# Kernel tuning notes

Measured on AMD Instinct MI355X. Metric: run time of the kernel, lower is better.

Reference implementation:

```python
import jax, jax.numpy as jnp
import numpy as np

EPS = 1e-6

def setup_inputs() -> dict:
    key = jax.random.key(0)
    kq, kk, kv = jax.random.split(key, 3)
    B, N, D = 4, 4096, 1024
    Q = jax.random.normal(kq, (B, N, D), dtype=jnp.float32)
    K = jax.random.normal(kk, (B, N, D), dtype=jnp.float32)
    V = jax.random.normal(kv, (B, N, D), dtype=jnp.float32)
    return {"Q": Q, "K": K, "V": V}

def reference(Q, K, V):
    # phi(x) = elu(x) + 1
    phi = lambda x: jax.nn.elu(x) + 1.0
    Q_phi = phi(Q)                                   # [B,N,D]
    K_phi = phi(K)                                   # [B,N,D]
    K_sum = K_phi.sum(axis=1)                        # [B,D]
    Z = jnp.einsum('bnd,bd->bn', Q_phi, K_sum) + EPS # [B,N]
    KV = jnp.einsum('bnd,bne->bde', K_phi, V)        # [B,D,E]
    context = jnp.einsum('bnd,bde->bne', Q_phi, KV)  # [B,N,E]
    out = context / Z[..., None]
    return out  # dropout is identity at inference (rate set to 0)
```

## Files before the change

kernel.cpp:

```cpp
#include <hip/hip_runtime.h>

#define BATCH 4
#define SEQ   4096
#define DIM   1024
#define EPS_F 1e-6f
#define KSPLIT 4

typedef __bf16 bf16_t;
typedef bf16_t bf16x8 __attribute__((ext_vector_type(8)));
typedef float  f32x4  __attribute__((ext_vector_type(4)));
typedef unsigned short u16x8 __attribute__((ext_vector_type(8)));

__device__ __forceinline__ unsigned short f2bf(float f) {
  unsigned u = __float_as_uint(f);
  u += 0x7FFFu + ((u >> 16) & 1u);
  return (unsigned short)(u >> 16);
}
__device__ __forceinline__ float bf2f(unsigned short h) {
  return __uint_as_float(((unsigned)h) << 16);
}
__device__ __forceinline__ float phi_f(float x) {
  return x > 0.f ? x + 1.f : __expf(x);
}

__global__ __launch_bounds__(256) void zero_f32(float* __restrict__ p, int n) {
  const int i = blockIdx.x * 256 + threadIdx.x;
  if (i < n) p[i] = 0.f;
}

template<bool PHI, bool KSUM>
__global__ __launch_bounds__(256) void phi_transpose(const float* __restrict__ in,
    unsigned short* __restrict__ out, float* __restrict__ ksum, int rows, int cols) {
  __shared__ float t[32][33];
  __shared__ float ps[8][32];
  const int bx = blockIdx.x * 32;
  const int by = blockIdx.y * 32;
  const size_t bo = (size_t)blockIdx.z * rows * cols;
  const int x = threadIdx.x, y = threadIdx.y;
  #pragma unroll
  for (int j = 0; j < 32; j += 8) {
    float v = in[bo + (size_t)(by + y + j) * cols + bx + x];
    if (PHI) v = phi_f(v);
    t[y + j][x] = v;
  }
  __syncthreads();
  #pragma unroll
  for (int j = 0; j < 32; j += 8)
    out[bo + (size_t)(bx + y + j) * rows + by + x] = f2bf(t[x][y + j]);
  if (KSUM) {
    float s = t[y][x] + t[y + 8][x] + t[y + 16][x] + t[y + 24][x];
    ps[y][x] = s;
    __syncthreads();
    if (y == 0) {
      float tot = 0.f;
      #pragma unroll
      for (int j = 0; j < 8; ++j) tot += ps[j][x];
      atomicAdd(&ksum[(size_t)blockIdx.z * cols + bx + x], tot);
    }
  }
}

__global__ __launch_bounds__(256) void phi_cast_qz(const float* __restrict__ Q,
    const float* __restrict__ Ksum, unsigned short* __restrict__ Qp,
    float* __restrict__ invZ) {
  const int row  = blockIdx.x * 4 + (threadIdx.x >> 6);
  const int lane = threadIdx.x & 63;
  const int b = row >> 12;
  const float* q  = Q + (size_t)row * DIM;
  const float* ks = Ksum + (size_t)b * DIM;
  float s = 0.f;
  #pragma unroll
  for (int c = 0; c < 2; ++c) {
    const int d0 = c * 512 + lane * 8;
    float4 v0 = *(const float4*)(q + d0);
    float4 v1 = *(const float4*)(q + d0 + 4);
    float4 k0 = *(const float4*)(ks + d0);
    float4 k1 = *(const float4*)(ks + d0 + 4);
    u16x8 o;
    o[0] = f2bf(phi_f(v0.x)); s += bf2f(o[0]) * k0.x;
    o[1] = f2bf(phi_f(v0.y)); s += bf2f(o[1]) * k0.y;
    o[2] = f2bf(phi_f(v0.z)); s += bf2f(o[2]) * k0.z;
    o[3] = f2bf(phi_f(v0.w)); s += bf2f(o[3]) * k0.w;
    o[4] = f2bf(phi_f(v1.x)); s += bf2f(o[4]) * k1.x;
    o[5] = f2bf(phi_f(v1.y)); s += bf2f(o[5]) * k1.y;
    o[6] = f2bf(phi_f(v1.z)); s += bf2f(o[6]) * k1.z;
    o[7] = f2bf(phi_f(v1.w)); s += bf2f(o[7]) * k1.w;
    *(u16x8*)(Qp + (size_t)row * DIM + d0) = o;
  }
  #pragma unroll
  for (int off = 32; off > 0; off >>= 1) s += __shfl_down(s, off);
  if (lane == 0) invZ[row] = 1.0f / (s + EPS_F);
}

__global__ __launch_bounds__(256) void reduce_kv(const unsigned short* __restrict__ P,
    unsigned short* __restrict__ KVt) {
  const size_t per = (size_t)DIM * DIM;
  const size_t i = ((size_t)blockIdx.x * 256 + threadIdx.x) * 8;
  const size_t b = blockIdx.y;
  const unsigned short* p = P + b * KSPLIT * per + i;
  float s[8] = {};
  #pragma unroll
  for (int sp = 0; sp < KSPLIT; ++sp) {
    u16x8 v = *(const u16x8*)(p + sp * per);
    #pragma unroll
    for (int j = 0; j < 8; ++j) s[j] += bf2f(v[j]);
  }
  u16x8 o;
  #pragma unroll
  for (int j = 0; j < 8; ++j) o[j] = f2bf(s[j]);
  *(u16x8*)(KVt + b * per + i) = o;
}

#define GLD(gp, lp) __builtin_amdgcn_global_load_lds( \
    (const __attribute__((address_space(1))) unsigned int*)(gp), \
    (__attribute__((address_space(3))) unsigned int*)(lp), 16, 0, 0)
#define BARRIER __builtin_amdgcn_s_barrier()
#define WAITV(n) asm volatile("s_waitcnt vmcnt(" #n ")" ::: "memory")

template<int EPI, int KS, int NT>
__global__ __launch_bounds__(512, 2) void gemm256_bt(
    const unsigned short* __restrict__ A, const unsigned short* __restrict__ Bm,
    void* __restrict__ Cv, const float* __restrict__ invZ,
    int M, int Nc, int K, int gx, int gy) {
  extern __shared__ unsigned short lds[];
  unsigned short* const As0 = lds;
  unsigned short* const As1 = lds + 16384;
  unsigned short* const Bs0 = lds + 32768;
  unsigned short* const Bs1 = lds + 49152;

  const int t    = threadIdx.x;
  const int wid  = t >> 6;
  const int lane = t & 63;
  const int id   = blockIdx.x;
  const int sw   = (id & 7) * (gridDim.x >> 3) + (id >> 3);
  const int bxi  = sw % gx;
  const int rem  = sw / gx;
  const int byi  = rem % gy;
  const int bz   = rem / gy;
  const int brow = byi * 256, bcol = bxi * 256;
  const size_t batch = bz / KS;
  const int split = bz % KS;
  const int Kc = K / KS;
  const unsigned short* Ab = A + batch * ((size_t)M * K) + (size_t)brow * K + (size_t)split * Kc;
  const unsigned short* Bb = Bm + batch * ((size_t)Nc * K) + (size_t)bcol * K + (size_t)split * Kc;

  const int srow_t = t >> 3;
  const int c_src  = (t & 7) ^ (srow_t & 7);
  const unsigned short* gA = Ab + (size_t)srow_t * K + c_src * 8;
  const unsigned short* gB = Bb + (size_t)((srow_t >> 5) * 64 + (srow_t & 31)) * K + c_src * 8;
  const int ldsAu = wid * 512;
  const int ldsBu = wid * 512 + (wid >> 2) * 2048;

  auto stageA = [&](unsigned short* D, int h, int kt) {
    GLD(gA + (size_t)(h * 64) * K + (size_t)kt * 64,       D + (h * 64) * 64 + ldsAu);
    GLD(gA + (size_t)(128 + h * 64) * K + (size_t)kt * 64, D + (128 + h * 64) * 64 + ldsAu);
  };
  auto stageB = [&](unsigned short* D, int h, int kt) {
    GLD(gB + (size_t)(h * 32) * K + (size_t)kt * 64,       D + (h * 32) * 64 + ldsBu);
    GLD(gB + (size_t)(128 + h * 32) * K + (size_t)kt * 64, D + (128 + h * 32) * 64 + ldsBu);
  };

  const int fr  = lane & 15;
  const int g   = lane >> 4;
  const int wrw = (wid >> 2) * 128;
  const int wcw = (wid & 3) * 64;
  const int ck0 = ((g)     ^ (fr & 7)) * 8;
  const int ck1 = ((4 + g) ^ (fr & 7)) * 8;

  f32x4 acc[8][4] = {};
  bf16x8 afX[4][2], afY[4][2], bfX[2][2], bfY[2][2];

#define LDA(S, mh, DST) { _Pragma("unroll") for (int m_ = 0; m_ < 4; ++m_) { \
    const int ro_ = (wrw + ((mh) * 4 + m_) * 16 + fr) * 64; \
    DST[m_][0] = *(const bf16x8*)((S) + ro_ + ck0); \
    DST[m_][1] = *(const bf16x8*)((S) + ro_ + ck1); } }
#define LDBF(S, nh, DST) { _Pragma("unroll") for (int n_ = 0; n_ < 2; ++n_) { \
    const int ro_ = (wcw + (nh) * 32 + n_ * 16 + fr) * 64; \
    DST[n_][0] = *(const bf16x8*)((S) + ro_ + ck0); \
    DST[n_][1] = *(const bf16x8*)((S) + ro_ + ck1); } }
#define MM(mh, nh, AF, BF) { __builtin_amdgcn_s_setprio(1); \
    _Pragma("unroll") for (int m_ = 0; m_ < 4; ++m_) \
    _Pragma("unroll") for (int n_ = 0; n_ < 2; ++n_) \
    _Pragma("unroll") for (int k_ = 0; k_ < 2; ++k_) \
      acc[(mh) * 4 + m_][(nh) * 2 + n_] = __builtin_amdgcn_mfma_f32_16x16x32_bf16( \
          AF[m_][k_], BF[n_][k_], acc[(mh) * 4 + m_][(nh) * 2 + n_], 0, 0, 0); \
    __builtin_amdgcn_s_setprio(0); }

  unsigned short *Ac = As0, *An = As1, *Bc = Bs0, *Bn = Bs1;

  stageA(Ac, 0, 0); stageB(Bc, 0, 0); stageB(Bc, 1, 0); stageA(Ac, 1, 0);
  stageA(An, 0, 1); stageB(Bn, 0, 1); stageB(Bn, 1, 1);
  stageA(An, 1, 1);
  WAITV(8);
  BARRIER;
  LDA(Ac, 0, afX); LDBF(Bc, 0, bfX);

  #pragma unroll 1
  for (int it = 0; it < NT - 2; ++it) {
    const int t2 = it + 2;
    LDBF(Bc, 1, bfY);
    stageA(Ac, 0, t2);
    BARRIER; MM(0, 0, afX, bfX); BARRIER;
    stageB(Bc, 0, t2);
    WAITV(6);
    BARRIER;
    LDA(Ac, 1, afY);
    MM(0, 1, afX, bfY); BARRIER;
    LDA(An, 0, afX);
    stageB(Bc, 1, t2);
    BARRIER; MM(1, 0, afY, bfX); BARRIER;
    LDBF(Bn, 0, bfX);
    stageA(Ac, 1, t2);
    BARRIER; MM(1, 1, afY, bfY); BARRIER;
    unsigned short* tp;
    tp = Ac; Ac = An; An = tp;
    tp = Bc; Bc = Bn; Bn = tp;
  }
  LDBF(Bc, 1, bfY);
  BARRIER; MM(0, 0, afX, bfX); BARRIER;
  WAITV(0);
  BARRIER;
  LDA(Ac, 1, afY);
  MM(0, 1, afX, bfY); BARRIER;
  LDA(An, 0, afX);
  BARRIER; MM(1, 0, afY, bfX); BARRIER;
  LDBF(Bn, 0, bfX);
  BARRIER; MM(1, 1, afY, bfY); BARRIER;
  {
    unsigned short* tp;
    tp = Ac; Ac = An; An = tp;
    tp = Bc; Bc = Bn; Bn = tp;
  }
  LDBF(Bc, 1, bfY);
  BARRIER; MM(0, 0, afX, bfX);
  LDA(Ac, 1, afY);
  MM(0, 1, afX, bfY);
  MM(1, 0, afY, bfX);
  MM(1, 1, afY, bfY);
#undef LDA
#undef LDBF
#undef MM

  if (EPI == 0) {
    unsigned short* Cb = (unsigned short*)Cv + (size_t)bz * M * Nc;
    #pragma unroll
    for (int m = 0; m < 8; ++m) {
      const int row = brow + wrw + m * 16 + g * 4;
      #pragma unroll
      for (int r = 0; r < 4; ++r)
        #pragma unroll
        for (int n = 0; n < 4; ++n)
          Cb[(size_t)(row + r) * Nc + bcol + wcw + n * 16 + fr] = f2bf(acc[m][n][r]);
    }
  } else {
    float* Cb = (float*)Cv + batch * ((size_t)M * Nc);
    const float* zb = invZ + batch * (size_t)M;
    #pragma unroll
    for (int m = 0; m < 8; ++m) {
      const int row = brow + wrw + m * 16 + g * 4;
      #pragma unroll
      for (int r = 0; r < 4; ++r) {
        const float z = zb[row + r];
        #pragma unroll
        for (int n = 0; n < 4; ++n)
          Cb[(size_t)(row + r) * Nc + bcol + wcw + n * 16 + fr] = acc[m][n][r] * z;
      }
    }
  }
}

extern "C" void kernel_launch(void* const* d_in, const int* in_sizes, int n_in,
                              void* d_out, int out_size, void* d_ws, size_t ws_size,
                              hipStream_t stream) {
  const float* Q = (const float*)d_in[0];
  const float* K = (const float*)d_in[1];
  const float* V = (const float*)d_in[2];
  float* out = (float*)d_out;

  char* ws = (char*)d_ws;
  size_t off = 0;
  auto alloc = [&](size_t bytes) {
    void* p = ws + off;
    off += (bytes + 255) & ~(size_t)255;
    return p;
  };
  unsigned short* Qp   = (unsigned short*)alloc((size_t)BATCH * SEQ * DIM * 2);
  unsigned short* P    = Qp;
  unsigned short* Kt   = (unsigned short*)alloc((size_t)BATCH * SEQ * DIM * 2);
  unsigned short* Vt   = (unsigned short*)alloc((size_t)BATCH * SEQ * DIM * 2);
  unsigned short* KVt  = (unsigned short*)alloc((size_t)BATCH * DIM * DIM * 2);
  float* Ksum = (float*)alloc((size_t)BATCH * DIM * 4);
  float* invZ = (float*)alloc((size_t)BATCH * SEQ * 4);

  hipFuncSetAttribute(reinterpret_cast<const void*>(&gemm256_bt<0, KSPLIT, 16>),
                      hipFuncAttributeMaxDynamicSharedMemorySize, 131072);
  hipFuncSetAttribute(reinterpret_cast<const void*>(&gemm256_bt<1, 1, 16>),
                      hipFuncAttributeMaxDynamicSharedMemorySize, 131072);

  const dim3 tb(32, 8);
  zero_f32<<<(BATCH * DIM + 255) / 256, 256, 0, stream>>>(Ksum, BATCH * DIM);
  phi_transpose<true, true ><<<dim3(DIM / 32, SEQ / 32, BATCH), tb, 0, stream>>>(K, Kt, Ksum, SEQ, DIM);
  phi_transpose<false, false><<<dim3(DIM / 32, SEQ / 32, BATCH), tb, 0, stream>>>(V, Vt, nullptr, SEQ, DIM);
  gemm256_bt<0, KSPLIT, 16><<<(DIM / 256) * (DIM / 256) * BATCH * KSPLIT, 512, 131072, stream>>>(
      Vt, Kt, P, nullptr, DIM, DIM, SEQ, DIM / 256, DIM / 256);
  reduce_kv<<<dim3(DIM * DIM / (256 * 8), BATCH), 256, 0, stream>>>(P, KVt);
  phi_cast_qz<<<BATCH * SEQ / 4, 256, 0, stream>>>(Q, Ksum, Qp, invZ);
  gemm256_bt<1, 1, 16><<<(DIM / 256) * (SEQ / 256) * BATCH, 512, 131072, stream>>>(
      Qp, KVt, out, invZ, SEQ, DIM, DIM, DIM / 256, SEQ / 256);
}
```

Baseline: 146.7 us.

## Fuse Q phi/bf16 conversion and normalizer into the second GEMM

Removes the separate phi_cast_qz pass. The second GEMM now loads fp32 Q directly, applies phi, converts to bf16 into LDS, and computes the Z normalizer in-kernel from a Ksum copy held in LDS. This avoids writing and re-reading the bf16 Qp buffer and drops one launch. In exchange, each of the 4 column tiles recomputes phi and Z for its rows and reads twice as many bytes of Q per tile. It also runs at occupancy 1 with extra LDS and more complex interleaving.

```diff
diff --git a/kernel.cpp b/kernel.cpp
--- a/kernel.cpp
+++ b/kernel.cpp
@@ -60,38 +60,6 @@
   }
 }
 
-__global__ __launch_bounds__(256) void phi_cast_qz(const float* __restrict__ Q,
-    const float* __restrict__ Ksum, unsigned short* __restrict__ Qp,
-    float* __restrict__ invZ) {
-  const int row  = blockIdx.x * 4 + (threadIdx.x >> 6);
-  const int lane = threadIdx.x & 63;
-  const int b = row >> 12;
-  const float* q  = Q + (size_t)row * DIM;
-  const float* ks = Ksum + (size_t)b * DIM;
-  float s = 0.f;
-  #pragma unroll
-  for (int c = 0; c < 2; ++c) {
-    const int d0 = c * 512 + lane * 8;
-    float4 v0 = *(const float4*)(q + d0);
-    float4 v1 = *(const float4*)(q + d0 + 4);
-    float4 k0 = *(const float4*)(ks + d0);
-    float4 k1 = *(const float4*)(ks + d0 + 4);
-    u16x8 o;
-    o[0] = f2bf(phi_f(v0.x)); s += bf2f(o[0]) * k0.x;
-    o[1] = f2bf(phi_f(v0.y)); s += bf2f(o[1]) * k0.y;
-    o[2] = f2bf(phi_f(v0.z)); s += bf2f(o[2]) * k0.z;
-    o[3] = f2bf(phi_f(v0.w)); s += bf2f(o[3]) * k0.w;
-    o[4] = f2bf(phi_f(v1.x)); s += bf2f(o[4]) * k1.x;
-    o[5] = f2bf(phi_f(v1.y)); s += bf2f(o[5]) * k1.y;
-    o[6] = f2bf(phi_f(v1.z)); s += bf2f(o[6]) * k1.z;
-    o[7] = f2bf(phi_f(v1.w)); s += bf2f(o[7]) * k1.w;
-    *(u16x8*)(Qp + (size_t)row * DIM + d0) = o;
-  }
-  #pragma unroll
-  for (int off = 32; off > 0; off >>= 1) s += __shfl_down(s, off);
-  if (lane == 0) invZ[row] = 1.0f / (s + EPS_F);
-}
-
 __global__ __launch_bounds__(256) void reduce_kv(const unsigned short* __restrict__ P,
     unsigned short* __restrict__ KVt) {
   const size_t per = (size_t)DIM * DIM;
@@ -116,6 +84,7 @@
     (__attribute__((address_space(3))) unsigned int*)(lp), 16, 0, 0)
 #define BARRIER __builtin_amdgcn_s_barrier()
 #define WAITV(n) asm volatile("s_waitcnt vmcnt(" #n ")" ::: "memory")
+#define LGK(n)   asm volatile("s_waitcnt lgkmcnt(" #n ")" ::: "memory")
 
 template<int EPI, int KS, int NT>
 __global__ __launch_bounds__(512, 2) void gemm256_bt(
@@ -269,6 +238,192 @@
   }
 }
 
+__global__ __launch_bounds__(512, 1) void gemm2f(
+    const float* __restrict__ Qf, const unsigned short* __restrict__ Bm,
+    float* __restrict__ C, const float* __restrict__ KsumG) {
+  extern __shared__ unsigned short lds[];
+  unsigned short* const As0 = lds;
+  unsigned short* const As1 = lds + 16384;
+  unsigned short* const Bs0 = lds + 32768;
+  unsigned short* const Bs1 = lds + 49152;
+  float* const ksumL = (float*)(lds + 65536);
+  float* const zbuf  = (float*)(lds + 32768);
+  float* const zfin  = ((float*)(lds + 32768)) + 2048;
+
+  const int t    = threadIdx.x;
+  const int wid  = t >> 6;
+  const int lane = t & 63;
+  const int id   = blockIdx.x;
+  const int sw   = (id & 7) * (gridDim.x >> 3) + (id >> 3);
+  const int bxi  = sw % 4;
+  const int rem  = sw / 4;
+  const int byi  = rem % 16;
+  const int bz   = rem / 16;
+  const int brow = byi * 256, bcol = bxi * 256;
+  const float*          Ab = Qf + (size_t)bz * SEQ * DIM + (size_t)brow * DIM;
+  const unsigned short* Bb = Bm + (size_t)bz * DIM * DIM + (size_t)bcol * DIM;
+
+  const int srow  = t >> 3;
+  const int c_src = (t & 7) ^ (srow & 7);
+  const float* gQ = Ab + (size_t)srow * DIM + c_src * 8;
+  const unsigned short* gB = Bb + (size_t)((srow >> 5) * 64 + (srow & 31)) * DIM + c_src * 8;
+  const int ldsBu = wid * 512 + (wid >> 2) * 2048;
+  const int aoff  = srow * 64 + (t & 7) * 8;
+
+  auto stageB = [&](unsigned short* D, int h, int kt) {
+    GLD(gB + (size_t)(h * 32) * DIM + (size_t)kt * 64,       D + (h * 32) * 64 + ldsBu);
+    GLD(gB + (size_t)(128 + h * 32) * DIM + (size_t)kt * 64, D + (128 + h * 32) * 64 + ldsBu);
+  };
+
+  const int fr  = lane & 15;
+  const int g   = lane >> 4;
+  const int wrw = (wid >> 2) * 128;
+  const int wcw = (wid & 3) * 64;
+  const int ck0 = ((g)     ^ (fr & 7)) * 8;
+  const int ck1 = ((4 + g) ^ (fr & 7)) * 8;
+
+  f32x4 acc[8][4] = {};
+  bf16x8 af[4][2], bf0[2][2], bf1[2][2];
+  float4 sA0, sA1, sA2, sA3, sB0, sB1, sB2, sB3;
+  float zp0 = 0.f, zp1 = 0.f, zp2 = 0.f, zp3 = 0.f;
+
+#define LOADA(S, mh) { _Pragma("unroll") for (int m_ = 0; m_ < 4; ++m_) { \
+    const int ro_ = (wrw + ((mh) * 4 + m_) * 16 + fr) * 64; \
+    af[m_][0] = *(const bf16x8*)((S) + ro_ + ck0); \
+    af[m_][1] = *(const bf16x8*)((S) + ro_ + ck1); } }
+#define LOADB(S, nh, BF) { _Pragma("unroll") for (int n_ = 0; n_ < 2; ++n_) { \
+    const int ro_ = (wcw + (nh) * 32 + n_ * 16 + fr) * 64; \
+    BF[n_][0] = *(const bf16x8*)((S) + ro_ + ck0); \
+    BF[n_][1] = *(const bf16x8*)((S) + ro_ + ck1); } }
+#define QUAD(mh, nh, BF) { __builtin_amdgcn_s_setprio(1); \
+    _Pragma("unroll") for (int m_ = 0; m_ < 4; ++m_) \
+    _Pragma("unroll") for (int n_ = 0; n_ < 2; ++n_) \
+    _Pragma("unroll") for (int k_ = 0; k_ < 2; ++k_) \
+      acc[(mh) * 4 + m_][(nh) * 2 + n_] = __builtin_amdgcn_mfma_f32_16x16x32_bf16( \
+          af[m_][k_], BF[n_][k_], acc[(mh) * 4 + m_][(nh) * 2 + n_], 0, 0, 0); \
+    __builtin_amdgcn_s_setprio(0); }
+#define ISSUEQ(P, h, kt) { \
+    P##0 = *(const float4*)(gQ + (size_t)((h) * 64) * DIM + (kt) * 64); \
+    P##1 = *(const float4*)(gQ + (size_t)((h) * 64) * DIM + (kt) * 64 + 4); \
+    P##2 = *(const float4*)(gQ + (size_t)((h) * 64 + 128) * DIM + (kt) * 64); \
+    P##3 = *(const float4*)(gQ + (size_t)((h) * 64 + 128) * DIM + (kt) * 64 + 4); }
+#define CVT8(VA, VB, OUT, ZP, K0, K1) { u16x8 o_; float q_; \
+    o_[0] = f2bf(phi_f(VA.x)); q_ = bf2f(o_[0]); ZP += q_ * K0.x; \
+    o_[1] = f2bf(phi_f(VA.y)); q_ = bf2f(o_[1]); ZP += q_ * K0.y; \
+    o_[2] = f2bf(phi_f(VA.z)); q_ = bf2f(o_[2]); ZP += q_ * K0.z; \
+    o_[3] = f2bf(phi_f(VA.w)); q_ = bf2f(o_[3]); ZP += q_ * K0.w; \
+    o_[4] = f2bf(phi_f(VB.x)); q_ = bf2f(o_[4]); ZP += q_ * K1.x; \
+    o_[5] = f2bf(phi_f(VB.y)); q_ = bf2f(o_[5]); ZP += q_ * K1.y; \
+    o_[6] = f2bf(phi_f(VB.z)); q_ = bf2f(o_[6]); ZP += q_ * K1.z; \
+    o_[7] = f2bf(phi_f(VB.w)); q_ = bf2f(o_[7]); ZP += q_ * K1.w; \
+    OUT = o_; }
+#define COMMITQ(P, D, h, kt, ZA, ZB) { \
+    float4 kv0 = *(const float4*)(ksumL + (kt) * 64 + c_src * 8); \
+    float4 kv1 = *(const float4*)(ksumL + (kt) * 64 + c_src * 8 + 4); \
+    u16x8 w0, w1; \
+    CVT8(P##0, P##1, w0, ZA, kv0, kv1); \
+    CVT8(P##2, P##3, w1, ZB, kv0, kv1); \
+    *(u16x8*)((D) + ((h) * 64) * 64 + aoff)         = w0; \
+    *(u16x8*)((D) + ((h) * 64 + 128) * 64 + aoff)   = w1; }
+
+  if (t < 128) {
+    float4 k0 = *(const float4*)(KsumG + (size_t)bz * DIM + t * 8);
+    float4 k1 = *(const float4*)(KsumG + (size_t)bz * DIM + t * 8 + 4);
+    *(float4*)(ksumL + t * 8) = k0;
+    *(float4*)(ksumL + t * 8 + 4) = k1;
+  }
+  __syncthreads();
+
+  ISSUEQ(sA, 0, 0);
+  ISSUEQ(sB, 1, 0);
+  stageB(Bs0, 0, 0); stageB(Bs0, 1, 0);
+  COMMITQ(sA, As0, 0, 0, zp0, zp2);
+  COMMITQ(sB, As0, 1, 0, zp1, zp3);
+  ISSUEQ(sA, 0, 1);
+  stageB(Bs1, 0, 1); stageB(Bs1, 1, 1);
+  COMMITQ(sA, As1, 0, 1, zp0, zp2);
+  LGK(0);
+  BARRIER;
+
+  #pragma unroll 1
+  for (int i = 0; i < 7; ++i) {
+    const int k2 = 2 * i;
+    LOADA(As0, 0); LOADB(Bs0, 0, bf0); ISSUEQ(sA, 1, k2 + 1);
+    BARRIER; QUAD(0, 0, bf0); BARRIER;
+    LOADB(Bs0, 1, bf1); ISSUEQ(sB, 0, k2 + 2);
+    BARRIER; QUAD(0, 1, bf1);
+    COMMITQ(sA, As1, 1, k2 + 1, zp1, zp3); LGK(0); BARRIER;
+    LOADA(As0, 1); stageB(Bs0, 0, k2 + 2);
+    BARRIER; QUAD(1, 0, bf0);
+    COMMITQ(sB, As0, 0, k2 + 2, zp0, zp2); LGK(0); BARRIER;
+    stageB(Bs0, 1, k2 + 2);
+    BARRIER; QUAD(1, 1, bf1); BARRIER;
+    LOADA(As1, 0); LOADB(Bs1, 0, bf0); ISSUEQ(sA, 1, k2 + 2);
+    BARRIER; QUAD(0, 0, bf0); BARRIER;
+    LOADB(Bs1, 1, bf1); ISSUEQ(sB, 0, k2 + 3);
+    BARRIER; QUAD(0, 1, bf1);
+    COMMITQ(sA, As0, 1, k2 + 2, zp1, zp3); LGK(0); BARRIER;
+    LOADA(As1, 1); stageB(Bs1, 0, k2 + 3);
+    BARRIER; QUAD(1, 0, bf0);
+    COMMITQ(sB, As1, 0, k2 + 3, zp0, zp2); LGK(0); BARRIER;
+    stageB(Bs1, 1, k2 + 3);
+    BARRIER; QUAD(1, 1, bf1); BARRIER;
+  }
+  {
+    LOADA(As0, 0); LOADB(Bs0, 0, bf0); ISSUEQ(sA, 1, 15);
+    BARRIER; QUAD(0, 0, bf0); BARRIER;
+    LOADB(Bs0, 1, bf1);
+    BARRIER; QUAD(0, 1, bf1);
+    COMMITQ(sA, As1, 1, 15, zp1, zp3); LGK(0); BARRIER;
+    LOADA(As0, 1);
+    BARRIER; QUAD(1, 0, bf0); BARRIER;
+    BARRIER; QUAD(1, 1, bf1); BARRIER;
+    LOADA(As1, 0); LOADB(Bs1, 0, bf0);
+    BARRIER; QUAD(0, 0, bf0); BARRIER;
+    LOADB(Bs1, 1, bf1);
+    BARRIER; QUAD(0, 1, bf1); BARRIER;
+    LOADA(As1, 1);
+    BARRIER; QUAD(1, 0, bf0); BARRIER;
+    QUAD(1, 1, bf1);
+  }
+#undef LOADA
+#undef LOADB
+#undef QUAD
+#undef ISSUEQ
+#undef CVT8
+#undef COMMITQ
+
+  BARRIER;
+  zbuf[(srow)       * 8 + (t & 7)] = zp0;
+  zbuf[(srow + 64)  * 8 + (t & 7)] = zp1;
+  zbuf[(srow + 128) * 8 + (t & 7)] = zp2;
+  zbuf[(srow + 192) * 8 + (t & 7)] = zp3;
+  LGK(0);
+  BARRIER;
+  if (t < 256) {
+    float4 a = *(const float4*)(zbuf + t * 8);
+    float4 b = *(const float4*)(zbuf + t * 8 + 4);
+    const float s = a.x + a.y + a.z + a.w + b.x + b.y + b.z + b.w;
+    zfin[t] = 1.0f / (s + EPS_F);
+  }
+  LGK(0);
+  BARRIER;
+
+  float* Cb = C + (size_t)bz * SEQ * DIM;
+  #pragma unroll
+  for (int m = 0; m < 8; ++m) {
+    const int rl = wrw + m * 16 + g * 4;
+    #pragma unroll
+    for (int r = 0; r < 4; ++r) {
+      const float z = zfin[rl + r];
+      const int row = brow + rl + r;
+      #pragma unroll
+      for (int n = 0; n < 4; ++n)
+        Cb[(size_t)row * DIM + bcol + wcw + n * 16 + fr] = acc[m][n][r] * z;
+    }
+  }
+}
+
 extern "C" void kernel_launch(void* const* d_in, const int* in_sizes, int n_in,
                               void* d_out, int out_size, void* d_ws, size_t ws_size,
                               hipStream_t stream) {
@@ -284,18 +439,16 @@
     off += (bytes + 255) & ~(size_t)255;
     return p;
   };
-  unsigned short* Qp   = (unsigned short*)alloc((size_t)BATCH * SEQ * DIM * 2);
-  unsigned short* P    = Qp;
+  unsigned short* P    = (unsigned short*)alloc((size_t)BATCH * KSPLIT * DIM * DIM * 2);
   unsigned short* Kt   = (unsigned short*)alloc((size_t)BATCH * SEQ * DIM * 2);
   unsigned short* Vt   = (unsigned short*)alloc((size_t)BATCH * SEQ * DIM * 2);
   unsigned short* KVt  = (unsigned short*)alloc((size_t)BATCH * DIM * DIM * 2);
   float* Ksum = (float*)alloc((size_t)BATCH * DIM * 4);
-  float* invZ = (float*)alloc((size_t)BATCH * SEQ * 4);
 
   hipFuncSetAttribute(reinterpret_cast<const void*>(&gemm256_bt<0, KSPLIT, 16>),
                       hipFuncAttributeMaxDynamicSharedMemorySize, 131072);
-  hipFuncSetAttribute(reinterpret_cast<const void*>(&gemm256_bt<1, 1, 16>),
-                      hipFuncAttributeMaxDynamicSharedMemorySize, 131072);
+  hipFuncSetAttribute(reinterpret_cast<const void*>(&gemm2f),
+                      hipFuncAttributeMaxDynamicSharedMemorySize, 135168);
 
   const dim3 tb(32, 8);
   zero_f32<<<(BATCH * DIM + 255) / 256, 256, 0, stream>>>(Ksum, BATCH * DIM);
@@ -304,7 +457,5 @@
   gemm256_bt<0, KSPLIT, 16><<<(DIM / 256) * (DIM / 256) * BATCH * KSPLIT, 512, 131072, stream>>>(
       Vt, Kt, P, nullptr, DIM, DIM, SEQ, DIM / 256, DIM / 256);
   reduce_kv<<<dim3(DIM * DIM / (256 * 8), BATCH), 256, 0, stream>>>(P, KVt);
-  phi_cast_qz<<<BATCH * SEQ / 4, 256, 0, stream>>>(Q, Ksum, Qp, invZ);
-  gemm256_bt<1, 1, 16><<<(DIM / 256) * (SEQ / 256) * BATCH, 512, 131072, stream>>>(
-      Qp, KVt, out, invZ, SEQ, DIM, DIM, DIM / 256, SEQ / 256);
-}
+  gemm2f<<<4 * 16 * BATCH, 512, 135168, stream>>>(Q, KVt, out, Ksum);
+}
```

Measured after the change: 251.5 us. 1.71x slower.

## Restructure 256x256 GEMM to 16 waves with simpler double-buffered loop

Applied to the files above, without the earlier changes.

Rewrites the bf16 GEMM to run 1024 threads (16 waves) per 256x256 tile, so each wave owns a 64x64 sub-tile with half the accumulators. The finely interleaved half-tile pipeline is replaced by one pass per k-step: read fragments, wait on all LDS and global loads, barrier, issue the next stage, then run all MFMAs. The intent is more waves to hide latency and lower per-wave register pressure. The cost is more LDS fragment reads per MFMA and full waitcnt(0) stalls each iteration. The zero kernel is also replaced with hipMemsetAsync.

```diff
diff --git a/kernel.cpp b/kernel.cpp
--- a/kernel.cpp
+++ b/kernel.cpp
@@ -23,15 +23,10 @@
   return x > 0.f ? x + 1.f : __expf(x);
 }
 
-__global__ __launch_bounds__(256) void zero_f32(float* __restrict__ p, int n) {
-  const int i = blockIdx.x * 256 + threadIdx.x;
-  if (i < n) p[i] = 0.f;
-}
-
 template<bool PHI, bool KSUM>
 __global__ __launch_bounds__(256) void phi_transpose(const float* __restrict__ in,
     unsigned short* __restrict__ out, float* __restrict__ ksum, int rows, int cols) {
-  __shared__ float t[32][33];
+  __shared__ float tl[32][33];
   __shared__ float ps[8][32];
   const int bx = blockIdx.x * 32;
   const int by = blockIdx.y * 32;
@@ -41,14 +36,14 @@
   for (int j = 0; j < 32; j += 8) {
     float v = in[bo + (size_t)(by + y + j) * cols + bx + x];
     if (PHI) v = phi_f(v);
-    t[y + j][x] = v;
+    tl[y + j][x] = v;
   }
   __syncthreads();
   #pragma unroll
   for (int j = 0; j < 32; j += 8)
-    out[bo + (size_t)(bx + y + j) * rows + by + x] = f2bf(t[x][y + j]);
+    out[bo + (size_t)(bx + y + j) * rows + by + x] = f2bf(tl[x][y + j]);
   if (KSUM) {
-    float s = t[y][x] + t[y + 8][x] + t[y + 16][x] + t[y + 24][x];
+    float s = tl[y][x] + tl[y + 8][x] + tl[y + 16][x] + tl[y + 24][x];
     ps[y][x] = s;
     __syncthreads();
     if (y == 0) {
@@ -116,9 +111,10 @@
     (__attribute__((address_space(3))) unsigned int*)(lp), 16, 0, 0)
 #define BARRIER __builtin_amdgcn_s_barrier()
 #define WAITV(n) asm volatile("s_waitcnt vmcnt(" #n ")" ::: "memory")
+#define LGK(n)   asm volatile("s_waitcnt lgkmcnt(" #n ")" ::: "memory")
 
 template<int EPI, int KS, int NT>
-__global__ __launch_bounds__(512, 2) void gemm256_bt(
+__global__ __launch_bounds__(1024, 4) void gemm16w(
     const unsigned short* __restrict__ A, const unsigned short* __restrict__ Bm,
     void* __restrict__ Cv, const float* __restrict__ invZ,
     int M, int Nc, int K, int gx, int gy) {
@@ -144,107 +140,85 @@
   const unsigned short* Ab = A + batch * ((size_t)M * K) + (size_t)brow * K + (size_t)split * Kc;
   const unsigned short* Bb = Bm + batch * ((size_t)Nc * K) + (size_t)bcol * K + (size_t)split * Kc;
 
-  const int srow_t = t >> 3;
-  const int c_src  = (t & 7) ^ (srow_t & 7);
-  const unsigned short* gA = Ab + (size_t)srow_t * K + c_src * 8;
-  const unsigned short* gB = Bb + (size_t)((srow_t >> 5) * 64 + (srow_t & 31)) * K + c_src * 8;
-  const int ldsAu = wid * 512;
-  const int ldsBu = wid * 512 + (wid >> 2) * 2048;
-
-  auto stageA = [&](unsigned short* D, int h, int kt) {
-    GLD(gA + (size_t)(h * 64) * K + (size_t)kt * 64,       D + (h * 64) * 64 + ldsAu);
-    GLD(gA + (size_t)(128 + h * 64) * K + (size_t)kt * 64, D + (128 + h * 64) * 64 + ldsAu);
+  const int srow  = t >> 3;
+  const int c_src = (t & 7) ^ (srow & 7);
+  const unsigned short* gA = Ab + (size_t)srow * K + c_src * 8;
+  const unsigned short* gB = Bb + (size_t)srow * K + c_src * 8;
+  const int ldsu = wid * 512;
+
+  auto stageA = [&](unsigned short* D, int kt) {
+    GLD(gA + (size_t)kt * 64,                  D + ldsu);
+    GLD(gA + (size_t)128 * K + (size_t)kt * 64, D + 8192 + ldsu);
   };
-  auto stageB = [&](unsigned short* D, int h, int kt) {
-    GLD(gB + (size_t)(h * 32) * K + (size_t)kt * 64,       D + (h * 32) * 64 + ldsBu);
-    GLD(gB + (size_t)(128 + h * 32) * K + (size_t)kt * 64, D + (128 + h * 32) * 64 + ldsBu);
+  auto stageB = [&](unsigned short* D, int kt) {
+    GLD(gB + (size_t)kt * 64,                  D + ldsu);
+    GLD(gB + (size_t)128 * K + (size_t)kt * 64, D + 8192 + ldsu);
   };
 
   const int fr  = lane & 15;
   const int g   = lane >> 4;
-  const int wrw = (wid >> 2) * 128;
+  const int wrw = (wid >> 2) * 64;
   const int wcw = (wid & 3) * 64;
   const int ck0 = ((g)     ^ (fr & 7)) * 8;
   const int ck1 = ((4 + g) ^ (fr & 7)) * 8;
 
-  f32x4 acc[8][4] = {};
-  bf16x8 afX[4][2], afY[4][2], bfX[2][2], bfY[2][2];
-
-#define LDA(S, mh, DST) { _Pragma("unroll") for (int m_ = 0; m_ < 4; ++m_) { \
-    const int ro_ = (wrw + ((mh) * 4 + m_) * 16 + fr) * 64; \
-    DST[m_][0] = *(const bf16x8*)((S) + ro_ + ck0); \
-    DST[m_][1] = *(const bf16x8*)((S) + ro_ + ck1); } }
-#define LDBF(S, nh, DST) { _Pragma("unroll") for (int n_ = 0; n_ < 2; ++n_) { \
-    const int ro_ = (wcw + (nh) * 32 + n_ * 16 + fr) * 64; \
-    DST[n_][0] = *(const bf16x8*)((S) + ro_ + ck0); \
-    DST[n_][1] = *(const bf16x8*)((S) + ro_ + ck1); } }
-#define MM(mh, nh, AF, BF) { __builtin_amdgcn_s_setprio(1); \
+  f32x4 acc[4][4] = {};
+  bf16x8 af[4][2], bfr[4][2];
+
+#define READS(SA, SB) { \
+    _Pragma("unroll") for (int m_ = 0; m_ < 4; ++m_) { \
+      const int ro_ = (wrw + m_ * 16 + fr) * 64; \
+      af[m_][0] = *(const bf16x8*)((SA) + ro_ + ck0); \
+      af[m_][1] = *(const bf16x8*)((SA) + ro_ + ck1); } \
+    _Pragma("unroll") for (int n_ = 0; n_ < 4; ++n_) { \
+      const int ro_ = (wcw + n_ * 16 + fr) * 64; \
+      bfr[n_][0] = *(const bf16x8*)((SB) + ro_ + ck0); \
+      bfr[n_][1] = *(const bf16x8*)((SB) + ro_ + ck1); } }
+#define MMALL { __builtin_amdgcn_s_setprio(1); \
     _Pragma("unroll") for (int m_ = 0; m_ < 4; ++m_) \
-    _Pragma("unroll") for (int n_ = 0; n_ < 2; ++n_) \
+    _Pragma("unroll") for (int n_ = 0; n_ < 4; ++n_) \
     _Pragma("unroll") for (int k_ = 0; k_ < 2; ++k_) \
-      acc[(mh) * 4 + m_][(nh) * 2 + n_] = __builtin_amdgcn_mfma_f32_16x16x32_bf16( \
-          AF[m_][k_], BF[n_][k_], acc[(mh) * 4 + m_][(nh) * 2 + n_], 0, 0, 0); \
+      acc[m_][n_] = __builtin_amdgcn_mfma_f32_16x16x32_bf16( \
+          af[m_][k_], bfr[n_][k_], acc[m_][n_], 0, 0, 0); \
     __builtin_amdgcn_s_setprio(0); }
 
   unsigned short *Ac = As0, *An = As1, *Bc = Bs0, *Bn = Bs1;
 
-  stageA(Ac, 0, 0); stageB(Bc, 0, 0); stageB(Bc, 1, 0); stageA(Ac, 1, 0);
-  stageA(An, 0, 1); stageB(Bn, 0, 1); stageB(Bn, 1, 1);
-  stageA(An, 1, 1);
-  WAITV(8);
+  stageA(Ac, 0); stageB(Bc, 0);
+  stageA(An, 1); stageB(Bn, 1);
+  WAITV(4);
   BARRIER;
-  LDA(Ac, 0, afX); LDBF(Bc, 0, bfX);
 
   #pragma unroll 1
-  for (int it = 0; it < NT - 2; ++it) {
-    const int t2 = it + 2;
-    LDBF(Bc, 1, bfY);
-    stageA(Ac, 0, t2);
-    BARRIER; MM(0, 0, afX, bfX); BARRIER;
-    stageB(Bc, 0, t2);
-    WAITV(6);
+  for (int kt = 0; kt < NT - 2; ++kt) {
+    READS(Ac, Bc);
+    LGK(0);
+    WAITV(0);
     BARRIER;
-    LDA(Ac, 1, afY);
-    MM(0, 1, afX, bfY); BARRIER;
-    LDA(An, 0, afX);
-    stageB(Bc, 1, t2);
-    BARRIER; MM(1, 0, afY, bfX); BARRIER;
-    LDBF(Bn, 0, bfX);
-    stageA(Ac, 1, t2);
-    BARRIER; MM(1, 1, afY, bfY); BARRIER;
+    stageA(Ac, kt + 2); stageB(Bc, kt + 2);
+    MMALL;
     unsigned short* tp;
     tp = Ac; Ac = An; An = tp;
     tp = Bc; Bc = Bn; Bn = tp;
   }
-  LDBF(Bc, 1, bfY);
-  BARRIER; MM(0, 0, afX, bfX); BARRIER;
-  WAITV(0);
-  BARRIER;
-  LDA(Ac, 1, afY);
-  MM(0, 1, afX, bfY); BARRIER;
-  LDA(An, 0, afX);
-  BARRIER; MM(1, 0, afY, bfX); BARRIER;
-  LDBF(Bn, 0, bfX);
-  BARRIER; MM(1, 1, afY, bfY); BARRIER;
+  READS(Ac, Bc);
+  LGK(0); WAITV(0); BARRIER;
+  MMALL;
   {
     unsigned short* tp;
     tp = Ac; Ac = An; An = tp;
     tp = Bc; Bc = Bn; Bn = tp;
   }
-  LDBF(Bc, 1, bfY);
-  BARRIER; MM(0, 0, afX, bfX);
-  LDA(Ac, 1, afY);
-  MM(0, 1, afX, bfY);
-  MM(1, 0, afY, bfX);
-  MM(1, 1, afY, bfY);
-#undef LDA
-#undef LDBF
-#undef MM
+  READS(Ac, Bc);
+  LGK(0);
+  MMALL;
+#undef READS
+#undef MMALL
 
   if (EPI == 0) {
     unsigned short* Cb = (unsigned short*)Cv + (size_t)bz * M * Nc;
     #pragma unroll
-    for (int m = 0; m < 8; ++m) {
+    for (int m = 0; m < 4; ++m) {
       const int row = brow + wrw + m * 16 + g * 4;
       #pragma unroll
       for (int r = 0; r < 4; ++r)
@@ -256,7 +230,7 @@
     float* Cb = (float*)Cv + batch * ((size_t)M * Nc);
     const float* zb = invZ + batch * (size_t)M;
     #pragma unroll
-    for (int m = 0; m < 8; ++m) {
+    for (int m = 0; m < 4; ++m) {
       const int row = brow + wrw + m * 16 + g * 4;
       #pragma unroll
       for (int r = 0; r < 4; ++r) {
@@ -292,19 +266,19 @@
   float* Ksum = (float*)alloc((size_t)BATCH * DIM * 4);
   float* invZ = (float*)alloc((size_t)BATCH * SEQ * 4);
 
-  hipFuncSetAttribute(reinterpret_cast<const void*>(&gemm256_bt<0, KSPLIT, 16>),
+  hipFuncSetAttribute(reinterpret_cast<const void*>(&gemm16w<0, KSPLIT, 16>),
                       hipFuncAttributeMaxDynamicSharedMemorySize, 131072);
-  hipFuncSetAttribute(reinterpret_cast<const void*>(&gemm256_bt<1, 1, 16>),
+  hipFuncSetAttribute(reinterpret_cast<const void*>(&gemm16w<1, 1, 16>),
                       hipFuncAttributeMaxDynamicSharedMemorySize, 131072);
 
   const dim3 tb(32, 8);
-  zero_f32<<<(BATCH * DIM + 255) / 256, 256, 0, stream>>>(Ksum, BATCH * DIM);
+  hipMemsetAsync(Ksum, 0, (size_t)BATCH * DIM * 4, stream);
   phi_transpose<true, true ><<<dim3(DIM / 32, SEQ / 32, BATCH), tb, 0, stream>>>(K, Kt, Ksum, SEQ, DIM);
   phi_transpose<false, false><<<dim3(DIM / 32, SEQ / 32, BATCH), tb, 0, stream>>>(V, Vt, nullptr, SEQ, DIM);
-  gemm256_bt<0, KSPLIT, 16><<<(DIM / 256) * (DIM / 256) * BATCH * KSPLIT, 512, 131072, stream>>>(
+  gemm16w<0, KSPLIT, 16><<<(DIM / 256) * (DIM / 256) * BATCH * KSPLIT, 1024, 131072, stream>>>(
       Vt, Kt, P, nullptr, DIM, DIM, SEQ, DIM / 256, DIM / 256);
   reduce_kv<<<dim3(DIM * DIM / (256 * 8), BATCH), 256, 0, stream>>>(P, KVt);
   phi_cast_qz<<<BATCH * SEQ / 4, 256, 0, stream>>>(Q, Ksum, Qp, invZ);
-  gemm256_bt<1, 1, 16><<<(DIM / 256) * (SEQ / 256) * BATCH, 512, 131072, stream>>>(
+  gemm16w<1, 1, 16><<<(DIM / 256) * (SEQ / 256) * BATCH, 1024, 131072, stream>>>(
       Qp, KVt, out, invZ, SEQ, DIM, DIM, DIM / 256, SEQ / 256);
 }
```

New measurement: 243.5 us. 65.9% more time.
